# Kernel tuning notes

Hardware: AMD Instinct MI355X
Metric: run time of the kernel (lower is better)

The kernel has to match this reference:

```python
import math
import jax, jax.numpy as jnp
import numpy as np

B, T, C, H, DQK, DV = 2, 2048, 1024, 16, 64, 64


def setup_inputs() -> dict:
    key = jax.random.key(0)
    ks = jax.random.split(key, 5)
    x = jax.random.normal(ks[0], (B, T, C), dtype=jnp.float32)
    # randw: randn(*d) / sqrt(d[-1])
    w_q = jax.random.normal(ks[1], (H, DQK, C), dtype=jnp.float32) / math.sqrt(C)
    w_k = jax.random.normal(ks[2], (H, DQK, C), dtype=jnp.float32) / math.sqrt(C)
    w_v = jax.random.normal(ks[3], (H, DV, C), dtype=jnp.float32) / math.sqrt(C)
    w_o = jax.random.normal(ks[4], (DV * H, C), dtype=jnp.float32) / math.sqrt(C)
    return {"x": x, "w_q": w_q, "w_k": w_k, "w_v": w_v, "w_o": w_o}


def reference(x, w_q, w_k, w_v, w_o):
    # Full-sequence causal forward (bs_q.first == 0, nb == T): caches are
    # fully written in one shot, so they reduce to the plain projections.
    n, t, c = x.shape
    q = jnp.einsum('ntc,hdc->nhtd', x, w_q)
    k = jnp.einsum('ntc,hdc->nhtd', x, w_k)
    v = jnp.einsum('ntc,hdc->nhtd', x, w_v)
    scale = 1.0 / math.sqrt(w_q.shape[1])
    a = jnp.einsum('nhtd,nhsd->nhts', q, k) * scale  # [n,h,t,s]
    causal = jnp.arange(t)[:, None] < jnp.arange(t)[None, :]  # True above diag
    a = jnp.where(causal[None, None, :, :], -jnp.inf, a)
    a = jax.nn.softmax(a, axis=3)
    y = jnp.einsum('nhts,nhsd->nthd', a, v).reshape(n, t, -1)  # [n,t,h*dv]
    return y @ w_o  # cache_y, [n,t,c]
```

## Files before the change

### kernel.cpp

```cpp
#include <hip/hip_runtime.h>


typedef short bf16x4 __attribute__((ext_vector_type(4)));
typedef short bf16x8 __attribute__((ext_vector_type(8)));
typedef float f32x4 __attribute__((ext_vector_type(4)));

#define MFMA_BF16 __builtin_amdgcn_mfma_f32_16x16x32_bf16

#define QSCALE 0.18033688011112042f

__device__ __forceinline__ unsigned short f2bf(float f) {
    union { float f; unsigned u; } un; un.f = f;
    unsigned r = un.u + 0x7fffu + ((un.u >> 16) & 1u);
    return (unsigned short)(r >> 16);
}
__device__ __forceinline__ unsigned pk2(float a, float b) {
    return (unsigned)f2bf(a) | ((unsigned)f2bf(b) << 16);
}
__device__ __forceinline__ unsigned pk2t(float a, float b) {
    union { float f; unsigned u; } ua, ub; ua.f = a; ub.f = b;
    return __builtin_amdgcn_perm(ub.u, ua.u, 0x07060302u);
}
__device__ __forceinline__ void gload16(const void* g, void* l) {
    __builtin_amdgcn_global_load_lds(
        (const __attribute__((address_space(1))) unsigned int*)g,
        (__attribute__((address_space(3))) unsigned int*)l, 16, 0, 0);
}

__global__ __launch_bounds__(256) void prep(
    const float* __restrict__ x, const float* __restrict__ wq,
    const float* __restrict__ wk, const float* __restrict__ wv,
    const float* __restrict__ wo,
    unsigned short* __restrict__ x16, unsigned short* __restrict__ wq16,
    unsigned short* __restrict__ wk16, unsigned short* __restrict__ wv16,
    unsigned short* __restrict__ wot)
{
    const int bid = blockIdx.x;
    if (bid < 3584) {
        const float* s; unsigned short* d; int off;
        if (bid < 2048)      { s = x;  d = x16;  off = bid * 2048; }
        else if (bid < 2560) { s = wq; d = wq16; off = (bid - 2048) * 2048; }
        else if (bid < 3072) { s = wk; d = wk16; off = (bid - 2560) * 2048; }
        else                 { s = wv; d = wv16; off = (bid - 3072) * 2048; }
        int i = off + threadIdx.x * 8;
        float4 f0 = *(const float4*)&s[i], f1 = *(const float4*)&s[i + 4];
        uint4 o;
        o.x = pk2(f0.x, f0.y); o.y = pk2(f0.z, f0.w);
        o.z = pk2(f1.x, f1.y); o.w = pk2(f1.z, f1.w);
        *(uint4*)&d[i] = o;
    } else {
        __shared__ unsigned short t[64 * 72];
        const int b2 = bid - 3584;
        const int k0 = (b2 & 15) << 6, n0 = (b2 >> 4) << 6;
        const int r = threadIdx.x >> 2, cg = (threadIdx.x & 3) << 4;
        const float* src = &wo[(k0 + r) * 1024 + n0 + cg];
        #pragma unroll
        for (int j = 0; j < 16; j += 4) {
            float4 f = *(const float4*)&src[j];
            t[(cg + j + 0) * 72 + r] = f2bf(f.x);
            t[(cg + j + 1) * 72 + r] = f2bf(f.y);
            t[(cg + j + 2) * 72 + r] = f2bf(f.z);
            t[(cg + j + 3) * 72 + r] = f2bf(f.w);
        }
        __syncthreads();
        unsigned short* dst = &wot[(n0 + r) * 1024 + k0 + cg];
        unsigned short* tr = &t[r * 72 + cg];
        unsigned v[16];
        #pragma unroll
        for (int j = 0; j < 16; ++j) v[j] = tr[j];
        uint4 o0, o1;
        o0.x = v[0] | (v[1] << 16);   o0.y = v[2] | (v[3] << 16);
        o0.z = v[4] | (v[5] << 16);   o0.w = v[6] | (v[7] << 16);
        o1.x = v[8] | (v[9] << 16);   o1.y = v[10] | (v[11] << 16);
        o1.z = v[12] | (v[13] << 16); o1.w = v[14] | (v[15] << 16);
        *(uint4*)&dst[0] = o0;
        *(uint4*)&dst[8] = o1;
    }
}

__device__ __forceinline__ void gemm_body(
    const unsigned short* __restrict__ A, const unsigned short* __restrict__ Bm,
    void* __restrict__ C, int m0, int n0, int mode, int ldc, float sc)
{
    __shared__ unsigned short sa[2][128 * 32];
    __shared__ unsigned short sb[2][128 * 32];
    const int tid = threadIdx.x, wave = tid >> 6, lane = tid & 63;
    const int l15 = lane & 15, l4 = lane >> 4;
    const int wm = (wave >> 1) << 6, wn = (wave & 1) << 6;

    const int r16 = lane >> 2;
    const int gcol = (((lane & 3) ^ ((r16 >> 1) & 3)) << 3);
    const int rcol = (l4 ^ ((l15 >> 1) & 3)) << 3;
    const unsigned short* Ag0 = &A[(size_t)(m0 + wave * 16 + r16) * 1024 + gcol];
    const unsigned short* Ag1 = Ag0 + (size_t)64 * 1024;
    const unsigned short* Bg0 = &Bm[(size_t)(n0 + wave * 16 + r16) * 1024 + gcol];
    const unsigned short* Bg1 = Bg0 + (size_t)64 * 1024;
    const int lb0 = (wave * 16) * 32;
    const int lb1 = (64 + wave * 16) * 32;

    gload16(Ag0, &sa[0][lb0]);
    gload16(Ag1, &sa[0][lb1]);
    gload16(Bg0, &sb[0][lb0]);
    gload16(Bg1, &sb[0][lb1]);
    __syncthreads();

    f32x4 acc[4][4] = {};

    #pragma unroll
    for (int kk = 0; kk < 32; ++kk) {
        const int cur = kk & 1;
        if (kk < 31) {
            const int off = (kk + 1) * 32;
            const int nxt = 1 - cur;
            gload16(Ag0 + off, &sa[nxt][lb0]);
            gload16(Ag1 + off, &sa[nxt][lb1]);
            gload16(Bg0 + off, &sb[nxt][lb0]);
            gload16(Bg1 + off, &sb[nxt][lb1]);
        }
        bf16x8 af[4], bf4[4];
        #pragma unroll
        for (int i = 0; i < 4; ++i)
            af[i] = *(const bf16x8*)&sa[cur][(wm + i * 16 + l15) * 32 + rcol];
        #pragma unroll
        for (int j = 0; j < 4; ++j)
            bf4[j] = *(const bf16x8*)&sb[cur][(wn + j * 16 + l15) * 32 + rcol];
        #pragma unroll
        for (int i = 0; i < 4; ++i)
            #pragma unroll
            for (int j = 0; j < 4; ++j)
                acc[i][j] = MFMA_BF16(af[i], bf4[j], acc[i][j], 0, 0, 0);
        __syncthreads();
    }

    #pragma unroll
    for (int i = 0; i < 4; ++i)
        #pragma unroll
        for (int j = 0; j < 4; ++j)
            #pragma unroll
            for (int r = 0; r < 4; ++r) {
                int row = m0 + wm + i * 16 + l4 * 4 + r;
                int col = n0 + wn + j * 16 + l15;
                float val = acc[i][j][r];
                if (mode == 0) {
                    int nb = row >> 11, t = row & 2047;
                    int hh = col >> 6, dd = col & 63;
                    ((unsigned short*)C)[(((nb << 4) + hh) * 2048 + t) * 64 + dd] =
                        f2bf(val * sc);
                } else if (mode == 1) {
                    ((float*)C)[(size_t)row * ldc + col] = val;
                } else {
                    int s = col & 31;
                    int cp = (col & ~31) | (((s >> 2) & 3) << 3)
                                         | (((s >> 4) & 1) << 2) | (s & 3);
                    ((unsigned short*)C)[(size_t)row * ldc + cp] = f2bf(val);
                }
            }
}

__global__ __launch_bounds__(256) void proj(
    const unsigned short* __restrict__ x16,
    const unsigned short* __restrict__ wq16,
    const unsigned short* __restrict__ wk16,
    const unsigned short* __restrict__ wv16,
    unsigned short* __restrict__ qbuf,
    unsigned short* __restrict__ kbuf,
    unsigned short* __restrict__ vtb)
{
    const int bid = blockIdx.x;
    if (bid < 512) {
        int m0 = (bid & 31) << 7;
        int n0g = (bid >> 5) << 7;
        if (n0g < 1024)
            gemm_body(x16, wq16, qbuf, m0, n0g, 0, 0, QSCALE);
        else
            gemm_body(x16, wk16, kbuf, m0, n0g - 1024, 0, 0, 1.0f);
    } else {
        int v = bid - 512;
        gemm_body(wv16, x16, vtb, (v & 7) << 7, (v >> 3) << 7, 2, 4096, 1.0f);
    }
}

__global__ __launch_bounds__(256) void outp(
    const unsigned short* __restrict__ ybuf,
    const unsigned short* __restrict__ wot,
    float* __restrict__ out)
{
    const int bid = blockIdx.x;
    gemm_body(ybuf, wot, out, (bid & 31) << 7, (bid >> 5) << 7, 1, 1024, 1.0f);
}

__global__ __launch_bounds__(512, 4) void attn(
    const unsigned short* __restrict__ q,
    const unsigned short* __restrict__ k,
    const unsigned short* __restrict__ vt,
    unsigned short* __restrict__ y)
{
    __shared__ unsigned short sk[2][2][64 * 64];
    __shared__ unsigned short sv[2][2][64 * 64];
    const int tid = threadIdx.x, wave = tid >> 6, lane = tid & 63;
    const int ws = wave & 3, wk2 = wave >> 2;
    const int l15 = lane & 15, l4 = lane >> 4;
    const int bid = blockIdx.x;
    const int qtt = (bid < 256) ? (15 - (bid >> 5)) : ((bid >> 5) - 8);
    const int bh = bid & 31;
    const int nb = bh >> 4, hh = bh & 15;
    const int q0 = qtt << 7;
    const size_t base = (size_t)bh << 17;

    const int lrow = lane >> 3;
    const int gch = ((lane & 7) ^ lrow) << 3;
    const int row = wave * 8 + lrow;
    const unsigned short* kg = &k[base + (size_t)row * 64 + gch];
    const unsigned short* vg = &vt[(size_t)((hh << 6) + row) * 4096 + (nb << 11) + gch];
    const int lb = (wave * 8) * 64;

    bf16x8 qf[2][2];
    #pragma unroll
    for (int g = 0; g < 2; ++g)
        #pragma unroll
        for (int ks = 0; ks < 2; ++ks)
            qf[g][ks] = *(const bf16x8*)
                &q[base + (size_t)(q0 + (g << 6) + ws * 16 + l15) * 64 + ks * 32 + l4 * 8];

    float l_sum[2] = {0.f, 0.f};
    f32x4 acc[2][4] = {};

    const int nsup = qtt + 1;

    const int rch0 = ((0 + l4) ^ (l15 & 7)) << 3;
    const int rch1 = ((4 + l4) ^ (l15 & 7)) << 3;

    auto stage_pair = [&](const int sbuf, const int p) {
        gload16(kg + ((size_t)p << 13),        &sk[sbuf][0][lb]);
        gload16(kg + ((size_t)p << 13) + 4096, &sk[sbuf][1][lb]);
        gload16(vg + (p << 7),      &sv[sbuf][0][lb]);
        gload16(vg + (p << 7) + 64, &sv[sbuf][1][lb]);
    };

    stage_pair(0, 0);
    __syncthreads();

    auto sstep = [&](const int cur, const int p) {
        if (p + 1 < nsup) stage_pair(cur ^ 1, p + 1);
        const int st = 2 * p + wk2;
        const unsigned short* skc = &sk[cur][wk2][0];
        const unsigned short* svc = &sv[cur][wk2][0];

        f32x4 s_acc[2][4] = {};
        #pragma unroll
        for (int ns = 0; ns < 4; ++ns) {
            bf16x8 kf0 = *(const bf16x8*)&skc[(ns * 16 + l15) * 64 + rch0];
            bf16x8 kf1 = *(const bf16x8*)&skc[(ns * 16 + l15) * 64 + rch1];
            s_acc[0][ns] = MFMA_BF16(kf0, qf[0][0], s_acc[0][ns], 0, 0, 0);
            s_acc[0][ns] = MFMA_BF16(kf1, qf[0][1], s_acc[0][ns], 0, 0, 0);
            s_acc[1][ns] = MFMA_BF16(kf0, qf[1][0], s_acc[1][ns], 0, 0, 0);
            s_acc[1][ns] = MFMA_BF16(kf1, qf[1][1], s_acc[1][ns], 0, 0, 0);
        }

        if (p == nsup - 1) {
            const int sb = st << 6;
            #pragma unroll
            for (int g = 0; g < 2; ++g) {
                const int qlg = q0 + (g << 6) + ws * 16 + l15;
                #pragma unroll
                for (int ns = 0; ns < 4; ++ns)
                    #pragma unroll
                    for (int r = 0; r < 4; ++r)
                        if (sb + ns * 16 + l4 * 4 + r > qlg) s_acc[g][ns][r] = -1e30f;
            }
        }

        float pe[2][4][4];
        #pragma unroll
        for (int g = 0; g < 2; ++g)
            #pragma unroll
            for (int ns = 0; ns < 4; ++ns) {
                #pragma unroll
                for (int r = 0; r < 4; ++r) pe[g][ns][r] = exp2f(s_acc[g][ns][r]);
                l_sum[g] += (pe[g][ns][0] + pe[g][ns][1]) + (pe[g][ns][2] + pe[g][ns][3]);
            }

        #pragma unroll
        for (int ks = 0; ks < 2; ++ks) {
            bf16x8 pf0, pf1;
            {
                uint4 pw;
                pw.x = pk2t(pe[0][2 * ks][0], pe[0][2 * ks][1]);
                pw.y = pk2t(pe[0][2 * ks][2], pe[0][2 * ks][3]);
                pw.z = pk2t(pe[0][2 * ks + 1][0], pe[0][2 * ks + 1][1]);
                pw.w = pk2t(pe[0][2 * ks + 1][2], pe[0][2 * ks + 1][3]);
                pf0 = *(bf16x8*)&pw;
            }
            {
                uint4 pw;
                pw.x = pk2t(pe[1][2 * ks][0], pe[1][2 * ks][1]);
                pw.y = pk2t(pe[1][2 * ks][2], pe[1][2 * ks][3]);
                pw.z = pk2t(pe[1][2 * ks + 1][0], pe[1][2 * ks + 1][1]);
                pw.w = pk2t(pe[1][2 * ks + 1][2], pe[1][2 * ks + 1][3]);
                pf1 = *(bf16x8*)&pw;
            }
            const int rch = ks ? rch1 : rch0;
            #pragma unroll
            for (int ds = 0; ds < 4; ++ds) {
                bf16x8 vf = *(const bf16x8*)&svc[(ds * 16 + l15) * 64 + rch];
                acc[0][ds] = MFMA_BF16(vf, pf0, acc[0][ds], 0, 0, 0);
                acc[1][ds] = MFMA_BF16(vf, pf1, acc[1][ds], 0, 0, 0);
            }
        }
        __syncthreads();
    };

    int p = 0;
    for (; p + 2 <= nsup; p += 2) {
        sstep(0, p);
        sstep(1, p + 1);
    }
    if (p < nsup) sstep(0, p);

    float* mrg = (float*)&sk[0][0][0];
    float* lsr = (float*)&sv[0][0][0];
    const int mb = ((ws << 6) + lane) << 5;
    if (wk2 == 1) {
        #pragma unroll
        for (int g = 0; g < 2; ++g)
            #pragma unroll
            for (int ds = 0; ds < 4; ++ds) {
                const int c = g * 4 + ds;
                *(f32x4*)&mrg[mb + ((c ^ (lane & 7)) << 2)] = acc[g][ds];
            }
        lsr[(((ws << 6) + lane) << 1) + 0] = l_sum[0];
        lsr[(((ws << 6) + lane) << 1) + 1] = l_sum[1];
    }
    __syncthreads();
    if (wk2 == 0) {
        #pragma unroll
        for (int g = 0; g < 2; ++g)
            #pragma unroll
            for (int ds = 0; ds < 4; ++ds) {
                const int c = g * 4 + ds;
                f32x4 o = *(const f32x4*)&mrg[mb + ((c ^ (lane & 7)) << 2)];
                acc[g][ds] += o;
            }
        l_sum[0] += lsr[(((ws << 6) + lane) << 1) + 0];
        l_sum[1] += lsr[(((ws << 6) + lane) << 1) + 1];

        #pragma unroll
        for (int g = 0; g < 2; ++g) {
            float ls = l_sum[g];
            ls += __shfl_xor(ls, 16);
            ls += __shfl_xor(ls, 32);
            const float rl = __builtin_amdgcn_rcpf(ls);

            const size_t rowbase =
                ((size_t)((nb << 11) + q0 + (g << 6) + ws * 16 + l15) << 10) + (hh << 6) + l4 * 4;
            #pragma unroll
            for (int ds = 0; ds < 4; ++ds) {
                uint2 o;
                o.x = pk2(acc[g][ds][0] * rl, acc[g][ds][1] * rl);
                o.y = pk2(acc[g][ds][2] * rl, acc[g][ds][3] * rl);
                *(uint2*)&y[rowbase + ds * 16] = o;
            }
        }
    }
}

extern "C" void kernel_launch(void* const* d_in, const int* in_sizes, int n_in,
                              void* d_out, int out_size, void* d_ws, size_t ws_size,
                              hipStream_t stream) {
    const float* x  = (const float*)d_in[0];
    const float* wq = (const float*)d_in[1];
    const float* wk = (const float*)d_in[2];
    const float* wv = (const float*)d_in[3];
    const float* wo = (const float*)d_in[4];
    float* out = (float*)d_out;

    const size_t M1 = 1u << 20;
    unsigned short* x16  = (unsigned short*)d_ws;
    unsigned short* wq16 = x16 + 4 * M1;
    unsigned short* wk16 = wq16 + M1;
    unsigned short* wv16 = wk16 + M1;
    unsigned short* wot  = wv16 + M1;
    unsigned short* qbuf = wot + M1;
    unsigned short* kbuf = qbuf + 4 * M1;
    unsigned short* vtb  = kbuf + 4 * M1;
    unsigned short* ybuf = vtb + 4 * M1;

    dim3 blk(256);
    prep<<<3840, blk, 0, stream>>>(x, wq, wk, wv, wo, x16, wq16, wk16, wv16, wot);
    proj<<<768, blk, 0, stream>>>(x16, wq16, wk16, wv16, qbuf, kbuf, vtb);
    attn<<<512, dim3(512), 0, stream>>>(qbuf, kbuf, vtb, ybuf);
    outp<<<256, blk, 0, stream>>>(ybuf, wot, out);
}
```

Measured before the change: 173.7 us.

## Balance causal attention work by pairing 64-row query tiles per block

Each attention block now handles two 64-row query tiles (t and 31-t) in sequence instead of one 128-row tile, so every block does about the same amount of causal work. Key blocks past the diagonal are skipped at 64-key granularity. The aim is to cut tail imbalance across blocks and avoid wasted masked compute. In exchange, each Q tile reuses the staged K/V less, the staging and merge barriers run twice per block, and the grid-size assumptions must match the launch.

Measured after the change: 169.1 us. -2.6%, faster.

```diff
diff --git a/kernel.cpp b/kernel.cpp
--- a/kernel.cpp
+++ b/kernel.cpp
@@ -201,10 +201,9 @@
     const int ws = wave & 3, wk2 = wave >> 2;
     const int l15 = lane & 15, l4 = lane >> 4;
     const int bid = blockIdx.x;
-    const int qtt = (bid < 256) ? (15 - (bid >> 5)) : ((bid >> 5) - 8);
+    const int pr = bid >> 5;
     const int bh = bid & 31;
     const int nb = bh >> 4, hh = bh & 15;
-    const int q0 = qtt << 7;
     const size_t base = (size_t)bh << 17;
 
     const int lrow = lane >> 3;
@@ -214,154 +213,127 @@
     const unsigned short* vg = &vt[(size_t)((hh << 6) + row) * 4096 + (nb << 11) + gch];
     const int lb = (wave * 8) * 64;
 
-    bf16x8 qf[2][2];
-    #pragma unroll
-    for (int g = 0; g < 2; ++g)
-        #pragma unroll
-        for (int ks = 0; ks < 2; ++ks)
-            qf[g][ks] = *(const bf16x8*)
-                &q[base + (size_t)(q0 + (g << 6) + ws * 16 + l15) * 64 + ks * 32 + l4 * 8];
-
-    float l_sum[2] = {0.f, 0.f};
-    f32x4 acc[2][4] = {};
-
-    const int nsup = qtt + 1;
-
     const int rch0 = ((0 + l4) ^ (l15 & 7)) << 3;
     const int rch1 = ((4 + l4) ^ (l15 & 7)) << 3;
 
-    auto stage_pair = [&](const int sbuf, const int p) {
-        gload16(kg + ((size_t)p << 13),        &sk[sbuf][0][lb]);
-        gload16(kg + ((size_t)p << 13) + 4096, &sk[sbuf][1][lb]);
-        gload16(vg + (p << 7),      &sv[sbuf][0][lb]);
-        gload16(vg + (p << 7) + 64, &sv[sbuf][1][lb]);
-    };
-
-    stage_pair(0, 0);
-    __syncthreads();
-
-    auto sstep = [&](const int cur, const int p) {
-        if (p + 1 < nsup) stage_pair(cur ^ 1, p + 1);
-        const int st = 2 * p + wk2;
-        const unsigned short* skc = &sk[cur][wk2][0];
-        const unsigned short* svc = &sv[cur][wk2][0];
-
-        f32x4 s_acc[2][4] = {};
-        #pragma unroll
-        for (int ns = 0; ns < 4; ++ns) {
-            bf16x8 kf0 = *(const bf16x8*)&skc[(ns * 16 + l15) * 64 + rch0];
-            bf16x8 kf1 = *(const bf16x8*)&skc[(ns * 16 + l15) * 64 + rch1];
-            s_acc[0][ns] = MFMA_BF16(kf0, qf[0][0], s_acc[0][ns], 0, 0, 0);
-            s_acc[0][ns] = MFMA_BF16(kf1, qf[0][1], s_acc[0][ns], 0, 0, 0);
-            s_acc[1][ns] = MFMA_BF16(kf0, qf[1][0], s_acc[1][ns], 0, 0, 0);
-            s_acc[1][ns] = MFMA_BF16(kf1, qf[1][1], s_acc[1][ns], 0, 0, 0);
-        }
-
-        if (p == nsup - 1) {
-            const int sb = st << 6;
-            #pragma unroll
-            for (int g = 0; g < 2; ++g) {
-                const int qlg = q0 + (g << 6) + ws * 16 + l15;
-                #pragma unroll
-                for (int ns = 0; ns < 4; ++ns)
-                    #pragma unroll
-                    for (int r = 0; r < 4; ++r)
-                        if (sb + ns * 16 + l4 * 4 + r > qlg) s_acc[g][ns][r] = -1e30f;
-            }
-        }
-
-        float pe[2][4][4];
-        #pragma unroll
-        for (int g = 0; g < 2; ++g)
-            #pragma unroll
-            for (int ns = 0; ns < 4; ++ns) {
-                #pragma unroll
-                for (int r = 0; r < 4; ++r) pe[g][ns][r] = exp2f(s_acc[g][ns][r]);
-                l_sum[g] += (pe[g][ns][0] + pe[g][ns][1]) + (pe[g][ns][2] + pe[g][ns][3]);
-            }
-
-        #pragma unroll
-        for (int ks = 0; ks < 2; ++ks) {
-            bf16x8 pf0, pf1;
-            {
-                uint4 pw;
-                pw.x = pk2t(pe[0][2 * ks][0], pe[0][2 * ks][1]);
-                pw.y = pk2t(pe[0][2 * ks][2], pe[0][2 * ks][3]);
-                pw.z = pk2t(pe[0][2 * ks + 1][0], pe[0][2 * ks + 1][1]);
-                pw.w = pk2t(pe[0][2 * ks + 1][2], pe[0][2 * ks + 1][3]);
-                pf0 = *(bf16x8*)&pw;
-            }
-            {
-                uint4 pw;
-                pw.x = pk2t(pe[1][2 * ks][0], pe[1][2 * ks][1]);
-                pw.y = pk2t(pe[1][2 * ks][2], pe[1][2 * ks][3]);
-                pw.z = pk2t(pe[1][2 * ks + 1][0], pe[1][2 * ks + 1][1]);
-                pw.w = pk2t(pe[1][2 * ks + 1][2], pe[1][2 * ks + 1][3]);
-                pf1 = *(bf16x8*)&pw;
-            }
-            const int rch = ks ? rch1 : rch0;
-            #pragma unroll
-            for (int ds = 0; ds < 4; ++ds) {
-                bf16x8 vf = *(const bf16x8*)&svc[(ds * 16 + l15) * 64 + rch];
-                acc[0][ds] = MFMA_BF16(vf, pf0, acc[0][ds], 0, 0, 0);
-                acc[1][ds] = MFMA_BF16(vf, pf1, acc[1][ds], 0, 0, 0);
-            }
-        }
-        __syncthreads();
-    };
-
-    int p = 0;
-    for (; p + 2 <= nsup; p += 2) {
-        sstep(0, p);
-        sstep(1, p + 1);
-    }
-    if (p < nsup) sstep(0, p);
-
     float* mrg = (float*)&sk[0][0][0];
     float* lsr = (float*)&sv[0][0][0];
-    const int mb = ((ws << 6) + lane) << 5;
-    if (wk2 == 1) {
-        #pragma unroll
-        for (int g = 0; g < 2; ++g)
-            #pragma unroll
-            for (int ds = 0; ds < 4; ++ds) {
-                const int c = g * 4 + ds;
-                *(f32x4*)&mrg[mb + ((c ^ (lane & 7)) << 2)] = acc[g][ds];
+    const int mslot = (ws << 6) + lane;
+    const int mb = mslot << 4;
+
+    auto process = [&](const int t) {
+        const int q0 = t << 6;
+        bf16x8 qf[2];
+        #pragma unroll
+        for (int ks = 0; ks < 2; ++ks)
+            qf[ks] = *(const bf16x8*)
+                &q[base + (size_t)(q0 + ws * 16 + l15) * 64 + ks * 32 + l4 * 8];
+
+        float l_sum = 0.f;
+        f32x4 acc[4] = {};
+        const int nsup = (t >> 1) + 1;
+
+        auto stage_pair = [&](const int sbuf, const int p) {
+            gload16(kg + ((size_t)p << 13), &sk[sbuf][0][lb]);
+            gload16(vg + (p << 7),          &sv[sbuf][0][lb]);
+            if (2 * p + 1 <= t) {
+                gload16(kg + ((size_t)p << 13) + 4096, &sk[sbuf][1][lb]);
+                gload16(vg + (p << 7) + 64,            &sv[sbuf][1][lb]);
             }
-        lsr[(((ws << 6) + lane) << 1) + 0] = l_sum[0];
-        lsr[(((ws << 6) + lane) << 1) + 1] = l_sum[1];
-    }
-    __syncthreads();
-    if (wk2 == 0) {
-        #pragma unroll
-        for (int g = 0; g < 2; ++g)
-            #pragma unroll
-            for (int ds = 0; ds < 4; ++ds) {
-                const int c = g * 4 + ds;
-                f32x4 o = *(const f32x4*)&mrg[mb + ((c ^ (lane & 7)) << 2)];
-                acc[g][ds] += o;
+        };
+
+        stage_pair(0, 0);
+        __syncthreads();
+
+        auto sstep = [&](const int cur, const int p) {
+            if (p + 1 < nsup) stage_pair(cur ^ 1, p + 1);
+            const int st = 2 * p + wk2;
+            if (st <= t) {
+                const unsigned short* skc = &sk[cur][wk2][0];
+                const unsigned short* svc = &sv[cur][wk2][0];
+
+                f32x4 s_acc[4] = {};
+                #pragma unroll
+                for (int ns = 0; ns < 4; ++ns) {
+                    bf16x8 kf0 = *(const bf16x8*)&skc[(ns * 16 + l15) * 64 + rch0];
+                    bf16x8 kf1 = *(const bf16x8*)&skc[(ns * 16 + l15) * 64 + rch1];
+                    s_acc[ns] = MFMA_BF16(kf0, qf[0], s_acc[ns], 0, 0, 0);
+                    s_acc[ns] = MFMA_BF16(kf1, qf[1], s_acc[ns], 0, 0, 0);
+                }
+
+                if (st == t) {
+                    const int ql = ws * 16 + l15;
+                    #pragma unroll
+                    for (int ns = 0; ns < 4; ++ns)
+                        #pragma unroll
+                        for (int r = 0; r < 4; ++r)
+                            if (ns * 16 + l4 * 4 + r > ql) s_acc[ns][r] = -1e30f;
+                }
+
+                float pe[4][4];
+                #pragma unroll
+                for (int ns = 0; ns < 4; ++ns) {
+                    #pragma unroll
+                    for (int r = 0; r < 4; ++r) pe[ns][r] = exp2f(s_acc[ns][r]);
+                    l_sum += (pe[ns][0] + pe[ns][1]) + (pe[ns][2] + pe[ns][3]);
+                }
+
+                #pragma unroll
+                for (int ks = 0; ks < 2; ++ks) {
+                    uint4 pw;
+                    pw.x = pk2t(pe[2 * ks][0], pe[2 * ks][1]);
+                    pw.y = pk2t(pe[2 * ks][2], pe[2 * ks][3]);
+                    pw.z = pk2t(pe[2 * ks + 1][0], pe[2 * ks + 1][1]);
+                    pw.w = pk2t(pe[2 * ks + 1][2], pe[2 * ks + 1][3]);
+                    bf16x8 pf = *(bf16x8*)&pw;
+                    const int rch = ks ? rch1 : rch0;
+                    #pragma unroll
+                    for (int ds = 0; ds < 4; ++ds) {
+                        bf16x8 vf = *(const bf16x8*)&svc[(ds * 16 + l15) * 64 + rch];
+                        acc[ds] = MFMA_BF16(vf, pf, acc[ds], 0, 0, 0);
+                    }
+                }
             }
-        l_sum[0] += lsr[(((ws << 6) + lane) << 1) + 0];
-        l_sum[1] += lsr[(((ws << 6) + lane) << 1) + 1];
-
-        #pragma unroll
-        for (int g = 0; g < 2; ++g) {
-            float ls = l_sum[g];
+            __syncthreads();
+        };
+
+        int p = 0;
+        for (; p + 2 <= nsup; p += 2) { sstep(0, p); sstep(1, p + 1); }
+        if (p < nsup) sstep(0, p);
+
+        if (wk2 == 1) {
+            #pragma unroll
+            for (int ds = 0; ds < 4; ++ds)
+                *(f32x4*)&mrg[mb + ((ds ^ (lane & 3)) << 2)] = acc[ds];
+            lsr[mslot] = l_sum;
+        }
+        __syncthreads();
+        if (wk2 == 0) {
+            #pragma unroll
+            for (int ds = 0; ds < 4; ++ds)
+                acc[ds] += *(const f32x4*)&mrg[mb + ((ds ^ (lane & 3)) << 2)];
+            l_sum += lsr[mslot];
+
+            float ls = l_sum;
             ls += __shfl_xor(ls, 16);
             ls += __shfl_xor(ls, 32);
             const float rl = __builtin_amdgcn_rcpf(ls);
 
             const size_t rowbase =
-                ((size_t)((nb << 11) + q0 + (g << 6) + ws * 16 + l15) << 10) + (hh << 6) + l4 * 4;
+                ((size_t)((nb << 11) + q0 + ws * 16 + l15) << 10) + (hh << 6) + l4 * 4;
             #pragma unroll
             for (int ds = 0; ds < 4; ++ds) {
                 uint2 o;
-                o.x = pk2(acc[g][ds][0] * rl, acc[g][ds][1] * rl);
-                o.y = pk2(acc[g][ds][2] * rl, acc[g][ds][3] * rl);
+                o.x = pk2(acc[ds][0] * rl, acc[ds][1] * rl);
+                o.y = pk2(acc[ds][2] * rl, acc[ds][3] * rl);
                 *(uint2*)&y[rowbase + ds * 16] = o;
             }
         }
-    }
+        __syncthreads();
+    };
+
+    process(31 - pr);
+    process(pr);
 }
 
 extern "C" void kernel_launch(void* const* d_in, const int* in_sizes, int n_in,
```

## Pair complementary causal query tiles per attention block for balanced work

Applied to the files above, without the earlier changes.

Each attention block now processes two query tiles, t and 15-t, one after the other, so every block does the same total number of key/value steps. The grid shrinks from 512 to 256 blocks and the launch-bounds occupancy hint drops from 4 to 2. The aim is to remove the load imbalance and tail effect of the causal mask, where some blocks ran 16 steps and others 1. The cost is fewer blocks in flight to hide latency, plus serialized work and an extra barrier inside each block.

Result: faster. 169.2 us (-2.6%).

```diff
diff --git a/kernel.cpp b/kernel.cpp
--- a/kernel.cpp
+++ b/kernel.cpp
@@ -189,7 +189,7 @@
     gemm_body(ybuf, wot, out, (bid & 31) << 7, (bid >> 5) << 7, 1, 1024, 1.0f);
 }
 
-__global__ __launch_bounds__(512, 4) void attn(
+__global__ __launch_bounds__(512, 2) void attn(
     const unsigned short* __restrict__ q,
     const unsigned short* __restrict__ k,
     const unsigned short* __restrict__ vt,
@@ -201,10 +201,9 @@
     const int ws = wave & 3, wk2 = wave >> 2;
     const int l15 = lane & 15, l4 = lane >> 4;
     const int bid = blockIdx.x;
-    const int qtt = (bid < 256) ? (15 - (bid >> 5)) : ((bid >> 5) - 8);
+    const int pr = bid >> 5;
     const int bh = bid & 31;
     const int nb = bh >> 4, hh = bh & 15;
-    const int q0 = qtt << 7;
     const size_t base = (size_t)bh << 17;
 
     const int lrow = lane >> 3;
@@ -214,154 +213,158 @@
     const unsigned short* vg = &vt[(size_t)((hh << 6) + row) * 4096 + (nb << 11) + gch];
     const int lb = (wave * 8) * 64;
 
-    bf16x8 qf[2][2];
-    #pragma unroll
-    for (int g = 0; g < 2; ++g)
-        #pragma unroll
-        for (int ks = 0; ks < 2; ++ks)
-            qf[g][ks] = *(const bf16x8*)
-                &q[base + (size_t)(q0 + (g << 6) + ws * 16 + l15) * 64 + ks * 32 + l4 * 8];
-
-    float l_sum[2] = {0.f, 0.f};
-    f32x4 acc[2][4] = {};
-
-    const int nsup = qtt + 1;
-
     const int rch0 = ((0 + l4) ^ (l15 & 7)) << 3;
     const int rch1 = ((4 + l4) ^ (l15 & 7)) << 3;
 
-    auto stage_pair = [&](const int sbuf, const int p) {
-        gload16(kg + ((size_t)p << 13),        &sk[sbuf][0][lb]);
-        gload16(kg + ((size_t)p << 13) + 4096, &sk[sbuf][1][lb]);
-        gload16(vg + (p << 7),      &sv[sbuf][0][lb]);
-        gload16(vg + (p << 7) + 64, &sv[sbuf][1][lb]);
-    };
-
-    stage_pair(0, 0);
-    __syncthreads();
-
-    auto sstep = [&](const int cur, const int p) {
-        if (p + 1 < nsup) stage_pair(cur ^ 1, p + 1);
-        const int st = 2 * p + wk2;
-        const unsigned short* skc = &sk[cur][wk2][0];
-        const unsigned short* svc = &sv[cur][wk2][0];
-
-        f32x4 s_acc[2][4] = {};
-        #pragma unroll
-        for (int ns = 0; ns < 4; ++ns) {
-            bf16x8 kf0 = *(const bf16x8*)&skc[(ns * 16 + l15) * 64 + rch0];
-            bf16x8 kf1 = *(const bf16x8*)&skc[(ns * 16 + l15) * 64 + rch1];
-            s_acc[0][ns] = MFMA_BF16(kf0, qf[0][0], s_acc[0][ns], 0, 0, 0);
-            s_acc[0][ns] = MFMA_BF16(kf1, qf[0][1], s_acc[0][ns], 0, 0, 0);
-            s_acc[1][ns] = MFMA_BF16(kf0, qf[1][0], s_acc[1][ns], 0, 0, 0);
-            s_acc[1][ns] = MFMA_BF16(kf1, qf[1][1], s_acc[1][ns], 0, 0, 0);
-        }
-
-        if (p == nsup - 1) {
-            const int sb = st << 6;
-            #pragma unroll
-            for (int g = 0; g < 2; ++g) {
-                const int qlg = q0 + (g << 6) + ws * 16 + l15;
-                #pragma unroll
-                for (int ns = 0; ns < 4; ++ns)
-                    #pragma unroll
-                    for (int r = 0; r < 4; ++r)
-                        if (sb + ns * 16 + l4 * 4 + r > qlg) s_acc[g][ns][r] = -1e30f;
-            }
-        }
-
-        float pe[2][4][4];
-        #pragma unroll
-        for (int g = 0; g < 2; ++g)
-            #pragma unroll
-            for (int ns = 0; ns < 4; ++ns) {
-                #pragma unroll
-                for (int r = 0; r < 4; ++r) pe[g][ns][r] = exp2f(s_acc[g][ns][r]);
-                l_sum[g] += (pe[g][ns][0] + pe[g][ns][1]) + (pe[g][ns][2] + pe[g][ns][3]);
-            }
-
-        #pragma unroll
-        for (int ks = 0; ks < 2; ++ks) {
-            bf16x8 pf0, pf1;
-            {
-                uint4 pw;
-                pw.x = pk2t(pe[0][2 * ks][0], pe[0][2 * ks][1]);
-                pw.y = pk2t(pe[0][2 * ks][2], pe[0][2 * ks][3]);
-                pw.z = pk2t(pe[0][2 * ks + 1][0], pe[0][2 * ks + 1][1]);
-                pw.w = pk2t(pe[0][2 * ks + 1][2], pe[0][2 * ks + 1][3]);
-                pf0 = *(bf16x8*)&pw;
-            }
-            {
-                uint4 pw;
-                pw.x = pk2t(pe[1][2 * ks][0], pe[1][2 * ks][1]);
-                pw.y = pk2t(pe[1][2 * ks][2], pe[1][2 * ks][3]);
-                pw.z = pk2t(pe[1][2 * ks + 1][0], pe[1][2 * ks + 1][1]);
-                pw.w = pk2t(pe[1][2 * ks + 1][2], pe[1][2 * ks + 1][3]);
-                pf1 = *(bf16x8*)&pw;
-            }
-            const int rch = ks ? rch1 : rch0;
-            #pragma unroll
-            for (int ds = 0; ds < 4; ++ds) {
-                bf16x8 vf = *(const bf16x8*)&svc[(ds * 16 + l15) * 64 + rch];
-                acc[0][ds] = MFMA_BF16(vf, pf0, acc[0][ds], 0, 0, 0);
-                acc[1][ds] = MFMA_BF16(vf, pf1, acc[1][ds], 0, 0, 0);
-            }
-        }
-        __syncthreads();
-    };
-
-    int p = 0;
-    for (; p + 2 <= nsup; p += 2) {
-        sstep(0, p);
-        sstep(1, p + 1);
-    }
-    if (p < nsup) sstep(0, p);
-
     float* mrg = (float*)&sk[0][0][0];
     float* lsr = (float*)&sv[0][0][0];
-    const int mb = ((ws << 6) + lane) << 5;
-    if (wk2 == 1) {
+    const int mslot = (ws << 6) + lane;
+    const int mb = mslot << 5;
+
+    auto process = [&](const int t) {
+        const int q0 = t << 7;
+        bf16x8 qf[2][2];
         #pragma unroll
         for (int g = 0; g < 2; ++g)
             #pragma unroll
-            for (int ds = 0; ds < 4; ++ds) {
-                const int c = g * 4 + ds;
-                *(f32x4*)&mrg[mb + ((c ^ (lane & 7)) << 2)] = acc[g][ds];
-            }
-        lsr[(((ws << 6) + lane) << 1) + 0] = l_sum[0];
-        lsr[(((ws << 6) + lane) << 1) + 1] = l_sum[1];
-    }
-    __syncthreads();
-    if (wk2 == 0) {
-        #pragma unroll
-        for (int g = 0; g < 2; ++g)
-            #pragma unroll
-            for (int ds = 0; ds < 4; ++ds) {
-                const int c = g * 4 + ds;
-                f32x4 o = *(const f32x4*)&mrg[mb + ((c ^ (lane & 7)) << 2)];
-                acc[g][ds] += o;
-            }
-        l_sum[0] += lsr[(((ws << 6) + lane) << 1) + 0];
-        l_sum[1] += lsr[(((ws << 6) + lane) << 1) + 1];
-
-        #pragma unroll
-        for (int g = 0; g < 2; ++g) {
-            float ls = l_sum[g];
-            ls += __shfl_xor(ls, 16);
-            ls += __shfl_xor(ls, 32);
-            const float rl = __builtin_amdgcn_rcpf(ls);
-
-            const size_t rowbase =
-                ((size_t)((nb << 11) + q0 + (g << 6) + ws * 16 + l15) << 10) + (hh << 6) + l4 * 4;
-            #pragma unroll
-            for (int ds = 0; ds < 4; ++ds) {
-                uint2 o;
-                o.x = pk2(acc[g][ds][0] * rl, acc[g][ds][1] * rl);
-                o.y = pk2(acc[g][ds][2] * rl, acc[g][ds][3] * rl);
-                *(uint2*)&y[rowbase + ds * 16] = o;
-            }
+            for (int ks = 0; ks < 2; ++ks)
+                qf[g][ks] = *(const bf16x8*)
+                    &q[base + (size_t)(q0 + (g << 6) + ws * 16 + l15) * 64 + ks * 32 + l4 * 8];
+
+        float l_sum[2] = {0.f, 0.f};
+        f32x4 acc[2][4] = {};
+        const int nsup = t + 1;
+
+        auto stage_pair = [&](const int sbuf, const int p) {
+            gload16(kg + ((size_t)p << 13),        &sk[sbuf][0][lb]);
+            gload16(kg + ((size_t)p << 13) + 4096, &sk[sbuf][1][lb]);
+            gload16(vg + (p << 7),      &sv[sbuf][0][lb]);
+            gload16(vg + (p << 7) + 64, &sv[sbuf][1][lb]);
+        };
+
+        stage_pair(0, 0);
+        __syncthreads();
+
+        auto sstep = [&](const int cur, const int p) {
+            if (p + 1 < nsup) stage_pair(cur ^ 1, p + 1);
+            const int st = 2 * p + wk2;
+            const unsigned short* skc = &sk[cur][wk2][0];
+            const unsigned short* svc = &sv[cur][wk2][0];
+
+            f32x4 s_acc[2][4] = {};
+            #pragma unroll
+            for (int ns = 0; ns < 4; ++ns) {
+                bf16x8 kf0 = *(const bf16x8*)&skc[(ns * 16 + l15) * 64 + rch0];
+                bf16x8 kf1 = *(const bf16x8*)&skc[(ns * 16 + l15) * 64 + rch1];
+                s_acc[0][ns] = MFMA_BF16(kf0, qf[0][0], s_acc[0][ns], 0, 0, 0);
+                s_acc[0][ns] = MFMA_BF16(kf1, qf[0][1], s_acc[0][ns], 0, 0, 0);
+                s_acc[1][ns] = MFMA_BF16(kf0, qf[1][0], s_acc[1][ns], 0, 0, 0);
+                s_acc[1][ns] = MFMA_BF16(kf1, qf[1][1], s_acc[1][ns], 0, 0, 0);
+            }
+
+            if (p == nsup - 1) {
+                const int sb = st << 6;
+                #pragma unroll
+                for (int g = 0; g < 2; ++g) {
+                    const int qlg = q0 + (g << 6) + ws * 16 + l15;
+                    #pragma unroll
+                    for (int ns = 0; ns < 4; ++ns)
+                        #pragma unroll
+                        for (int r = 0; r < 4; ++r)
+                            if (sb + ns * 16 + l4 * 4 + r > qlg) s_acc[g][ns][r] = -1e30f;
+                }
+            }
+
+            float pe[2][4][4];
+            #pragma unroll
+            for (int g = 0; g < 2; ++g)
+                #pragma unroll
+                for (int ns = 0; ns < 4; ++ns) {
+                    #pragma unroll
+                    for (int r = 0; r < 4; ++r) pe[g][ns][r] = exp2f(s_acc[g][ns][r]);
+                    l_sum[g] += (pe[g][ns][0] + pe[g][ns][1]) + (pe[g][ns][2] + pe[g][ns][3]);
+                }
+
+            #pragma unroll
+            for (int ks = 0; ks < 2; ++ks) {
+                bf16x8 pf0, pf1;
+                {
+                    uint4 pw;
+                    pw.x = pk2t(pe[0][2 * ks][0], pe[0][2 * ks][1]);
+                    pw.y = pk2t(pe[0][2 * ks][2], pe[0][2 * ks][3]);
+                    pw.z = pk2t(pe[0][2 * ks + 1][0], pe[0][2 * ks + 1][1]);
+                    pw.w = pk2t(pe[0][2 * ks + 1][2], pe[0][2 * ks + 1][3]);
+                    pf0 = *(bf16x8*)&pw;
+                }
+                {
+                    uint4 pw;
+                    pw.x = pk2t(pe[1][2 * ks][0], pe[1][2 * ks][1]);
+                    pw.y = pk2t(pe[1][2 * ks][2], pe[1][2 * ks][3]);
+                    pw.z = pk2t(pe[1][2 * ks + 1][0], pe[1][2 * ks + 1][1]);
+                    pw.w = pk2t(pe[1][2 * ks + 1][2], pe[1][2 * ks + 1][3]);
+                    pf1 = *(bf16x8*)&pw;
+                }
+                const int rch = ks ? rch1 : rch0;
+                #pragma unroll
+                for (int ds = 0; ds < 4; ++ds) {
+                    bf16x8 vf = *(const bf16x8*)&svc[(ds * 16 + l15) * 64 + rch];
+                    acc[0][ds] = MFMA_BF16(vf, pf0, acc[0][ds], 0, 0, 0);
+                    acc[1][ds] = MFMA_BF16(vf, pf1, acc[1][ds], 0, 0, 0);
+                }
+            }
+            __syncthreads();
+        };
+
+        int p = 0;
+        for (; p + 2 <= nsup; p += 2) { sstep(0, p); sstep(1, p + 1); }
+        if (p < nsup) sstep(0, p);
+
+        if (wk2 == 1) {
+            #pragma unroll
+            for (int g = 0; g < 2; ++g)
+                #pragma unroll
+                for (int ds = 0; ds < 4; ++ds) {
+                    const int c = g * 4 + ds;
+                    *(f32x4*)&mrg[mb + ((c ^ (lane & 7)) << 2)] = acc[g][ds];
+                }
+            lsr[(mslot << 1) + 0] = l_sum[0];
+            lsr[(mslot << 1) + 1] = l_sum[1];
         }
-    }
+        __syncthreads();
+        if (wk2 == 0) {
+            #pragma unroll
+            for (int g = 0; g < 2; ++g)
+                #pragma unroll
+                for (int ds = 0; ds < 4; ++ds) {
+                    const int c = g * 4 + ds;
+                    acc[g][ds] += *(const f32x4*)&mrg[mb + ((c ^ (lane & 7)) << 2)];
+                }
+            l_sum[0] += lsr[(mslot << 1) + 0];
+            l_sum[1] += lsr[(mslot << 1) + 1];
+
+            #pragma unroll
+            for (int g = 0; g < 2; ++g) {
+                float ls = l_sum[g];
+                ls += __shfl_xor(ls, 16);
+                ls += __shfl_xor(ls, 32);
+                const float rl = __builtin_amdgcn_rcpf(ls);
+
+                const size_t rowbase =
+                    ((size_t)((nb << 11) + q0 + (g << 6) + ws * 16 + l15) << 10) + (hh << 6) + l4 * 4;
+                #pragma unroll
+                for (int ds = 0; ds < 4; ++ds) {
+                    uint2 o;
+                    o.x = pk2(acc[g][ds][0] * rl, acc[g][ds][1] * rl);
+                    o.y = pk2(acc[g][ds][2] * rl, acc[g][ds][3] * rl);
+                    *(uint2*)&y[rowbase + ds * 16] = o;
+                }
+            }
+        }
+        __syncthreads();
+    };
+
+    process(15 - pr);
+    process(pr);
 }
 
 extern "C" void kernel_launch(void* const* d_in, const int* in_sizes, int n_in,
@@ -388,6 +391,6 @@
     dim3 blk(256);
     prep<<<3840, blk, 0, stream>>>(x, wq, wk, wv, wo, x16, wq16, wk16, wv16, wot);
     proj<<<768, blk, 0, stream>>>(x16, wq16, wk16, wv16, qbuf, kbuf, vtb);
-    attn<<<512, dim3(512), 0, stream>>>(qbuf, kbuf, vtb, ybuf);
+    attn<<<256, dim3(512), 0, stream>>>(qbuf, kbuf, vtb, ybuf);
     outp<<<256, blk, 0, stream>>>(ybuf, wot, out);
 }
```
